# Kernel tuning notes

Hardware: AMD Instinct MI355X
Metric: run time of the kernel (lower is better)

## Reference

```python
import jax, jax.numpy as jnp
import numpy as np

B, T, F, E = 256, 256, 8, 128
H = 2 * E  # hidden_dim = 2*embedding_dim = 256
NL = 5     # num_layers per LSTM stack


def setup_inputs() -> dict:
    key = jax.random.key(0)
    ks = jax.random.split(key, 9)
    s1 = 1.0 / np.sqrt(H)
    s2 = 1.0 / np.sqrt(E)
    u = lambda k, shape, s: jax.random.uniform(k, shape, jnp.float32, -s, s)
    return {
        "x": jax.random.normal(ks[0], (B, T, F), jnp.float32),
        # stack 1: input F -> hidden H, 5 layers. b = b_ih + b_hh combined.
        "w_ih0_1": u(ks[1], (4 * H, F), s1),
        "w_ihr_1": u(ks[2], (NL - 1, 4 * H, H), s1),
        "w_hh_1": u(ks[3], (NL, 4 * H, H), s1),
        "b_1": u(ks[4], (NL, 4 * H), s1),
        # stack 2: input H -> hidden E, 5 layers
        "w_ih0_2": u(ks[5], (4 * E, H), s2),
        "w_ihr_2": u(ks[6], (NL - 1, 4 * E, E), s2),
        "w_hh_2": u(ks[7], (NL, 4 * E, E), s2),
        "b_2": u(ks[8], (NL, 4 * E), s2),
    }


def _lstm_layer(x, w_ih, w_hh, b):
    """x: [B,T,D] -> (outputs [B,T,Hd], final hidden [B,Hd]). PyTorch gate order i,f,g,o."""
    Hd = w_hh.shape[-1]
    # precompute input contribution for all timesteps (the big GEMM)
    xg = jnp.einsum('btd,gd->tbg', x, w_ih) + b  # [T,B,4Hd]
    h0 = jnp.zeros((x.shape[0], Hd), x.dtype)

    def step(carry, xt):
        h, c = carry
        g = xt + h @ w_hh.T
        i, f, gg, o = jnp.split(g, 4, axis=-1)
        c = jax.nn.sigmoid(f) * c + jax.nn.sigmoid(i) * jnp.tanh(gg)
        h = jax.nn.sigmoid(o) * jnp.tanh(c)
        return (h, c), h

    (h, _), hs = jax.lax.scan(step, (h0, h0), xg)
    return jnp.swapaxes(hs, 0, 1), h


def _stack(x, w_ih0, w_ihr, w_hh, b):
    y, h = _lstm_layer(x, w_ih0, w_hh[0], b[0])
    for l in range(1, w_hh.shape[0]):
        y, h = _lstm_layer(y, w_ihr[l - 1], w_hh[l], b[l])
    return y, h


def reference(x, w_ih0_1, w_ihr_1, w_hh_1, b_1, w_ih0_2, w_ihr_2, w_hh_2, b_2):
    x = x.reshape(x.shape[0], T, F)
    y, _ = _stack(x, w_ih0_1, w_ihr_1, w_hh_1, b_1)   # [B,T,H]
    _, h = _stack(y, w_ih0_2, w_ihr_2, w_hh_2, b_2)   # h: [B,E] last layer final hidden
    return h
```

## Files before the change

### kernel.cpp

```cpp
#include <hip/hip_runtime.h>
#include <math.h>

typedef unsigned short u16;
typedef unsigned int   u32;
typedef unsigned long long u64;
typedef __bf16 bf16x8 __attribute__((ext_vector_type(8)));
typedef float  f32x4  __attribute__((ext_vector_type(4)));

#define BB 256
#define TT 256
#define HD 256
#define ED 128
#define NSTEPS 265

#define H_U32   (10 * 2 * BB * HD)
#define CTR_OFF H_U32
#define CTR_U32 512
#define XP_OFF  (H_U32 + CTR_U32)
#define XP_U32  (BB * TT * 8)
#define WT_OFF  (XP_OFF + XP_U32)

__constant__ size_t g_woff[10] = {0ul,589824ul,1638400ul,2686976ul,3735552ul,
                                  4784128ul,5177344ul,5439488ul,5701632ul,5963776ul};
__constant__ int g_cb[11] = {0,73728,204800,335872,466944,598016,
                             647168,679936,712704,745472,778240};

__device__ __forceinline__ u16 f2bf_hi(float f) {
    u32 u = __float_as_uint(f);
    u32 r = (u + 0x7FFFu + ((u >> 16) & 1u)) >> 16;
    return (u16)r;
}
__device__ __forceinline__ float bf2f(u16 h) { return __uint_as_float(((u32)h) << 16); }
__device__ __forceinline__ float sigmoidf_(float v) { return 1.0f / (1.0f + expf(-v)); }

__global__ __launch_bounds__(256) void zero_state(u32* wsd) {
    const int n = XP_OFF;
    for (int i = blockIdx.x * blockDim.x + threadIdx.x; i < n; i += gridDim.x * blockDim.x)
        wsd[i] = 0u;
}

__global__ __launch_bounds__(256) void conv_x(const float* __restrict__ x, u32* __restrict__ wsd) {
    u32* xp = wsd + XP_OFF;
    for (int i = blockIdx.x * blockDim.x + threadIdx.x; i < XP_U32; i += gridDim.x * blockDim.x) {
        float v = x[i];
        u16 hi = f2bf_hi(v);
        u16 lo = f2bf_hi(v - bf2f(hi));
        xp[i] = (u32)hi | ((u32)lo << 16);
    }
}

__global__ __launch_bounds__(256) void conv_all(
    const float* __restrict__ w_ih0_1, const float* __restrict__ w_ihr_1,
    const float* __restrict__ w_hh_1,
    const float* __restrict__ w_ih0_2, const float* __restrict__ w_ihr_2,
    const float* __restrict__ w_hh_2,
    u32* __restrict__ wsd)
{
    __bf16* dst0 = (__bf16*)(wsd + WT_OFF);
    const int nch = 778240;
    for (int ci = blockIdx.x * blockDim.x + threadIdx.x; ci < nch;
         ci += gridDim.x * blockDim.x) {
        int l = 0;
        while (ci >= g_cb[l + 1]) ++l;
        int di = ci - g_cb[l];

        const int hd  = (l < 5) ? 256 : 128;
        const int din = (l == 0) ? 32 : ((l < 6) ? 256 : 128);
        const int xw  = (l == 0) ? 8 : din;
        const int Kp  = din + hd;
        const int nk  = Kp >> 5;

        const float *wih, *whh; int wihld, whhld;
        if (l == 0)      { wih = w_ih0_1;                                whh = w_hh_1;
                           wihld = 8;   whhld = 256; }
        else if (l < 5)  { wih = w_ihr_1 + (size_t)(l - 1) * 1024 * 256; whh = w_hh_1 + (size_t)l * 1024 * 256;
                           wihld = 256; whhld = 256; }
        else if (l == 5) { wih = w_ih0_2;                                whh = w_hh_2;
                           wihld = 256; whhld = 128; }
        else             { wih = w_ihr_2 + (size_t)(l - 6) * 512 * 128;  whh = w_hh_2 + (size_t)(l - 5) * 512 * 128;
                           wihld = 128; whhld = 128; }

        int lane = di & 63;
        int rem  = di >> 6;
        int kt   = rem % nk;
        int rem2 = rem / nk;
        int p    = rem2 & 1;
        int g    = (rem2 >> 1) & 3;
        int jt   = rem2 >> 3;
        int r15  = lane & 15, kq = lane >> 4;
        int row  = g * hd + jt * 16 + r15;

        bf16x8 o8;
        #pragma unroll
        for (int e = 0; e < 8; ++e) {
            int k = kt * 32 + kq * 8 + e;
            float v = 0.0f;
            if (k < xw) v = wih[(size_t)row * wihld + k];
            else if (k >= din && k < Kp) v = whh[(size_t)row * whhld + (k - din)];
            __bf16 h = (__bf16)v;
            o8[e] = p ? (__bf16)(v - (float)h) : h;
        }
        *(bf16x8*)(dst0 + g_woff[l] + (size_t)di * 8) = o8;
    }
}

__device__ __forceinline__ void unpack8(const uint4& a, const uint4& b, bf16x8& bh, bf16x8& bl) {
    union { u32 u[4]; bf16x8 v; } H, L;
    H.u[0] = (a.x & 0xFFFFu) | (a.y << 16);
    H.u[1] = (a.z & 0xFFFFu) | (a.w << 16);
    H.u[2] = (b.x & 0xFFFFu) | (b.y << 16);
    H.u[3] = (b.z & 0xFFFFu) | (b.w << 16);
    L.u[0] = (a.x >> 16) | (a.y & 0xFFFF0000u);
    L.u[1] = (a.z >> 16) | (a.w & 0xFFFF0000u);
    L.u[2] = (b.x >> 16) | (b.y & 0xFFFF0000u);
    L.u[3] = (b.z >> 16) | (b.w & 0xFFFF0000u);
    bh = H.v; bl = L.v;
}

template<int NKI, int NKT, bool ISL0>
__device__ void run_persist(int l, int bid, int xcd, int jt, int bt, int hd,
    const float* __restrict__ bias, u32* __restrict__ hbuf, u32* __restrict__ ctr,
    const u32* __restrict__ xp, float* __restrict__ out, const u16* __restrict__ A_sh)
{
    constexpr int DIN = NKI * 32;
    constexpr int RD  = (NKT < 8) ? NKT : 8;

    const int tid  = threadIdx.x;
    const int lane = tid & 63;
    const int wv   = tid >> 6;
    const int r15  = lane & 15;
    const int kq   = lane >> 4;
    const int brow = bt * 128 + wv * 16 + r15;
    const int j0   = jt * 16 + kq * 4;

    float bgr[4][4];
    #pragma unroll
    for (int g = 0; g < 4; ++g) {
        float4 v = *(const float4*)&bias[g * hd + j0];
        bgr[g][0] = v.x; bgr[g][1] = v.y; bgr[g][2] = v.z; bgr[g][3] = v.w;
    }

    int offH[4], offL[4];
    #pragma unroll
    for (int g = 0; g < 4; ++g) {
        offH[g] = (g * 2)     * NKT * 512 + lane * 8;
        offL[g] = (g * 2 + 1) * NKT * 512 + lane * 8;
    }

    float4 cv = make_float4(0.f, 0.f, 0.f, 0.f);
    const int lm = (l > 0) ? (l - 1) : 0;

    for (int w = 0; w < NSTEPS; ++w) {
        const int t = w - l;
        if (t >= 0 && t < TT) {
            const u32* hin   = hbuf + ((size_t)lm * 2 + (t & 1)) * (BB * HD);
            const u32* hprev = hbuf + ((size_t)l * 2 + ((t & 1) ^ 1)) * (BB * HD);
            u32*       hout  = hbuf + ((size_t)l * 2 + (t & 1)) * (BB * HD);

            auto ldB = [&](int kt, uint4& A, uint4& B) {
                if constexpr (ISL0) {
                    if (kt == 0) {
                        if (kq == 0) {
                            const uint4* p = (const uint4*)(xp + ((size_t)brow * TT + t) * 8);
                            A = p[0]; B = p[1];
                        } else { A = make_uint4(0,0,0,0); B = make_uint4(0,0,0,0); }
                    } else {
                        const u32* p = hprev + (size_t)brow * HD + (kt * 32 - 32) + kq * 8;
                        A = *(const uint4*)p; B = *(const uint4*)(p + 4);
                    }
                } else {
                    const int k0 = kt * 32 + kq * 8;
                    const u32* p = (kt < NKI) ? (hin + (size_t)brow * HD + k0)
                                              : (hprev + (size_t)brow * HD + (k0 - DIN));
                    A = *(const uint4*)p; B = *(const uint4*)(p + 4);
                }
            };

            f32x4 acc0 = {0.f,0.f,0.f,0.f}, acc1 = {0.f,0.f,0.f,0.f};
            f32x4 acc2 = {0.f,0.f,0.f,0.f}, acc3 = {0.f,0.f,0.f,0.f};

            uint4 rA[RD], rB[RD];
            #pragma unroll
            for (int i = 0; i < RD; ++i) ldB(i, rA[i], rB[i]);

            #pragma unroll
            for (int kt = 0; kt < NKT; ++kt) {
                bf16x8 bh, bl;
                unpack8(rA[kt % RD], rB[kt % RD], bh, bl);
                if (kt + RD < NKT) ldB(kt + RD, rA[kt % RD], rB[kt % RD]);

                const int kof = kt * 512;
                bf16x8 a0h = *(const bf16x8*)&A_sh[offH[0] + kof];
                bf16x8 a1h = *(const bf16x8*)&A_sh[offH[1] + kof];
                bf16x8 a2h = *(const bf16x8*)&A_sh[offH[2] + kof];
                bf16x8 a3h = *(const bf16x8*)&A_sh[offH[3] + kof];
                bf16x8 a0l = *(const bf16x8*)&A_sh[offL[0] + kof];
                bf16x8 a1l = *(const bf16x8*)&A_sh[offL[1] + kof];
                bf16x8 a2l = *(const bf16x8*)&A_sh[offL[2] + kof];
                bf16x8 a3l = *(const bf16x8*)&A_sh[offL[3] + kof];

                acc0 = __builtin_amdgcn_mfma_f32_16x16x32_bf16(a0h, bh, acc0, 0, 0, 0);
                acc1 = __builtin_amdgcn_mfma_f32_16x16x32_bf16(a1h, bh, acc1, 0, 0, 0);
                acc2 = __builtin_amdgcn_mfma_f32_16x16x32_bf16(a2h, bh, acc2, 0, 0, 0);
                acc3 = __builtin_amdgcn_mfma_f32_16x16x32_bf16(a3h, bh, acc3, 0, 0, 0);
                acc0 = __builtin_amdgcn_mfma_f32_16x16x32_bf16(a0h, bl, acc0, 0, 0, 0);
                acc1 = __builtin_amdgcn_mfma_f32_16x16x32_bf16(a1h, bl, acc1, 0, 0, 0);
                acc2 = __builtin_amdgcn_mfma_f32_16x16x32_bf16(a2h, bl, acc2, 0, 0, 0);
                acc3 = __builtin_amdgcn_mfma_f32_16x16x32_bf16(a3h, bl, acc3, 0, 0, 0);
                acc0 = __builtin_amdgcn_mfma_f32_16x16x32_bf16(a0l, bh, acc0, 0, 0, 0);
                acc1 = __builtin_amdgcn_mfma_f32_16x16x32_bf16(a1l, bh, acc1, 0, 0, 0);
                acc2 = __builtin_amdgcn_mfma_f32_16x16x32_bf16(a2l, bh, acc2, 0, 0, 0);
                acc3 = __builtin_amdgcn_mfma_f32_16x16x32_bf16(a3l, bh, acc3, 0, 0, 0);
            }

            float4 hv;
            {
                float i_, f_, g_, o_;
                i_ = sigmoidf_(acc0[0] + bgr[0][0]); f_ = sigmoidf_(acc1[0] + bgr[1][0]);
                g_ = tanhf   (acc2[0] + bgr[2][0]); o_ = sigmoidf_(acc3[0] + bgr[3][0]);
                cv.x = fmaf(f_, cv.x, i_ * g_); hv.x = o_ * tanhf(cv.x);
                i_ = sigmoidf_(acc0[1] + bgr[0][1]); f_ = sigmoidf_(acc1[1] + bgr[1][1]);
                g_ = tanhf   (acc2[1] + bgr[2][1]); o_ = sigmoidf_(acc3[1] + bgr[3][1]);
                cv.y = fmaf(f_, cv.y, i_ * g_); hv.y = o_ * tanhf(cv.y);
                i_ = sigmoidf_(acc0[2] + bgr[0][2]); f_ = sigmoidf_(acc1[2] + bgr[1][2]);
                g_ = tanhf   (acc2[2] + bgr[2][2]); o_ = sigmoidf_(acc3[2] + bgr[3][2]);
                cv.z = fmaf(f_, cv.z, i_ * g_); hv.z = o_ * tanhf(cv.z);
                i_ = sigmoidf_(acc0[3] + bgr[0][3]); f_ = sigmoidf_(acc1[3] + bgr[1][3]);
                g_ = tanhf   (acc2[3] + bgr[2][3]); o_ = sigmoidf_(acc3[3] + bgr[3][3]);
                cv.w = fmaf(f_, cv.w, i_ * g_); hv.w = o_ * tanhf(cv.w);
            }

            u32 pk0, pk1, pk2, pk3;
            {
                u16 h0 = f2bf_hi(hv.x); pk0 = (u32)h0 | ((u32)f2bf_hi(hv.x - bf2f(h0)) << 16);
                u16 h1 = f2bf_hi(hv.y); pk1 = (u32)h1 | ((u32)f2bf_hi(hv.y - bf2f(h1)) << 16);
                u16 h2 = f2bf_hi(hv.z); pk2 = (u32)h2 | ((u32)f2bf_hi(hv.z - bf2f(h2)) << 16);
                u16 h3 = f2bf_hi(hv.w); pk3 = (u32)h3 | ((u32)f2bf_hi(hv.w - bf2f(h3)) << 16);
            }
            u64* hp = (u64*)(hout + (size_t)brow * HD + j0);
            __hip_atomic_store(hp + 0, (u64)pk0 | ((u64)pk1 << 32), __ATOMIC_RELAXED, __HIP_MEMORY_SCOPE_AGENT);
            __hip_atomic_store(hp + 1, (u64)pk2 | ((u64)pk3 << 32), __ATOMIC_RELAXED, __HIP_MEMORY_SCOPE_AGENT);

            if (l == 9 && t == TT - 1)
                *(float4*)&out[(size_t)brow * ED + j0] = hv;
        }

        __syncthreads();
        if (tid == 0) {
            __hip_atomic_fetch_add(&ctr[xcd * 32], 1u,
                                   __ATOMIC_RELAXED, __HIP_MEMORY_SCOPE_AGENT);
            const u32 w1 = (u32)(w + 1);
            if (bid == 0) {
                for (int it = 0; it < (1 << 22); ++it) {
                    bool ok = true;
                    #pragma unroll
                    for (int r = 0; r < 8; ++r) {
                        u32 tgt = ((r == 7) ? 16u : 32u) * w1;
                        ok &= (__hip_atomic_load(&ctr[r * 32], __ATOMIC_RELAXED,
                                                 __HIP_MEMORY_SCOPE_AGENT) >= tgt);
                    }
                    if (ok) break;
                    __builtin_amdgcn_s_sleep(1);
                }
                __hip_atomic_store(&ctr[256], w1, __ATOMIC_RELAXED, __HIP_MEMORY_SCOPE_AGENT);
            } else {
                for (int it = 0; it < (1 << 22); ++it) {
                    if (__hip_atomic_load(&ctr[256], __ATOMIC_RELAXED,
                                          __HIP_MEMORY_SCOPE_AGENT) >= w1) break;
                    __builtin_amdgcn_s_sleep(1);
                }
            }
            __builtin_amdgcn_fence(__ATOMIC_ACQUIRE, "agent");
        }
        __syncthreads();
    }
}

__global__ __launch_bounds__(512, 2) void lstm_persist(
    const float* __restrict__ b_1, const float* __restrict__ b_2,
    u32* __restrict__ wsd, float* __restrict__ out)
{
    __shared__ __align__(16) u16 A_sh[65536];

    const int bid = blockIdx.x;
    const int xcd = bid & 7, slot = bid >> 3;
    int l, jt, bt;
    if (xcd < 5)      { l = xcd;               bt = slot >> 4;        jt = slot & 15; }
    else if (xcd == 5){ l = 5 + (slot >> 4);   bt = (slot >> 3) & 1;  jt = slot & 7; }
    else if (xcd == 6){ l = 7 + (slot >> 4);   bt = (slot >> 3) & 1;  jt = slot & 7; }
    else              { if (slot >= 16) return; l = 9; bt = slot >> 3; jt = slot & 7; }

    const int hd  = (l < 5) ? 256 : 128;
    const int din = (l == 0) ? 32 : ((l < 6) ? 256 : 128);
    const int nk  = (din + hd) >> 5;
    const float* bias = (l < 5) ? (b_1 + l * 1024) : (b_2 + (l - 5) * 512);

    u32* hbuf = wsd;
    u32* ctr  = wsd + CTR_OFF;
    const u32* xp = wsd + XP_OFF;
    const u16* wt = (const u16*)(wsd + WT_OFF);

    {
        const uint4* src = (const uint4*)(wt + g_woff[l] + (size_t)jt * 8 * nk * 512);
        uint4* dst = (uint4*)A_sh;
        const int n4 = nk * 512;
        for (int i = threadIdx.x; i < n4; i += 512) dst[i] = src[i];
    }
    __syncthreads();

    if (l == 0)
        run_persist<1, 9, true >(l, bid, xcd, jt, bt, hd, bias, hbuf, ctr, xp, out, A_sh);
    else if (l < 5)
        run_persist<8, 16, false>(l, bid, xcd, jt, bt, hd, bias, hbuf, ctr, xp, out, A_sh);
    else if (l == 5)
        run_persist<8, 12, false>(l, bid, xcd, jt, bt, hd, bias, hbuf, ctr, xp, out, A_sh);
    else
        run_persist<4, 8, false>(l, bid, xcd, jt, bt, hd, bias, hbuf, ctr, xp, out, A_sh);
}

extern "C" void kernel_launch(void* const* d_in, const int* in_sizes, int n_in,
                              void* d_out, int out_size, void* d_ws, size_t ws_size,
                              hipStream_t stream) {
    const float* x       = (const float*)d_in[0];
    const float* w_ih0_1 = (const float*)d_in[1];
    const float* w_ihr_1 = (const float*)d_in[2];
    const float* w_hh_1  = (const float*)d_in[3];
    const float* b_1     = (const float*)d_in[4];
    const float* w_ih0_2 = (const float*)d_in[5];
    const float* w_ihr_2 = (const float*)d_in[6];
    const float* w_hh_2  = (const float*)d_in[7];
    const float* b_2     = (const float*)d_in[8];
    u32*   wsd = (u32*)d_ws;
    float* out = (float*)d_out;

    hipLaunchKernelGGL(zero_state, dim3(1024), dim3(256), 0, stream, wsd);
    hipLaunchKernelGGL(conv_all, dim3(1024), dim3(256), 0, stream,
                       w_ih0_1, w_ihr_1, w_hh_1, w_ih0_2, w_ihr_2, w_hh_2, wsd);
    hipLaunchKernelGGL(conv_x, dim3(256), dim3(256), 0, stream, x, wsd);
    hipLaunchKernelGGL(lstm_persist, dim3(256), dim3(512), 0, stream,
                       b_1, b_2, wsd, out);
}
```

Before: 3.286 ms.

## Replace per-step global barrier with paired steps and per-group flag sync

Each global-barrier epoch now runs two timesteps per layer, with a lightweight per-(layer,batch-tile) group counter synchronising the blocks that share a recurrence between the two steps. The hidden-state ring buffer grows from depth 2 to 4 so that layers skewed by two steps can read inputs without overwriting them. The aim is to roughly halve the number of expensive grid-wide barriers. In exchange it adds a second sync point per epoch, deeper buffering in workspace, and a prefetch depth reduced from 8 to 4.

```diff
diff --git a/kernel.cpp b/kernel.cpp
--- a/kernel.cpp
+++ b/kernel.cpp
@@ -11,12 +11,13 @@
 #define TT 256
 #define HD 256
 #define ED 128
-#define NSTEPS 265
-
-#define H_U32   (10 * 2 * BB * HD)
+#define DEPTH 4
+#define NE 137
+
+#define H_U32   (10 * DEPTH * BB * HD)
 #define CTR_OFF H_U32
-#define CTR_U32 512
-#define XP_OFF  (H_U32 + CTR_U32)
+#define GRP_OFF (CTR_OFF + 512)
+#define XP_OFF  (GRP_OFF + 640)
 #define XP_U32  (BB * TT * 8)
 #define WT_OFF  (XP_OFF + XP_U32)
 
@@ -118,20 +119,21 @@
 }
 
 template<int NKI, int NKT, bool ISL0>
-__device__ void run_persist(int l, int bid, int xcd, int jt, int bt, int hd,
+__device__ void run_persist(int l, int bid, int xcd, int jt, int bt, int hd, u32 arr7,
+    int nblkg, u32* __restrict__ gflg,
     const float* __restrict__ bias, u32* __restrict__ hbuf, u32* __restrict__ ctr,
     const u32* __restrict__ xp, float* __restrict__ out, const u16* __restrict__ A_sh)
 {
     constexpr int DIN = NKI * 32;
-    constexpr int RD  = (NKT < 8) ? NKT : 8;
+    constexpr int RS  = (NKT < 4) ? NKT : 4;
 
     const int tid  = threadIdx.x;
     const int lane = tid & 63;
     const int wv   = tid >> 6;
     const int r15  = lane & 15;
-    const int kq   = lane >> 4;
+    const int kqc  = lane >> 4;
     const int brow = bt * 128 + wv * 16 + r15;
-    const int j0   = jt * 16 + kq * 4;
+    const int j0   = jt * 16 + kqc * 4;
 
     float bgr[4][4];
     #pragma unroll
@@ -150,112 +152,132 @@
     float4 cv = make_float4(0.f, 0.f, 0.f, 0.f);
     const int lm = (l > 0) ? (l - 1) : 0;
 
-    for (int w = 0; w < NSTEPS; ++w) {
-        const int t = w - l;
-        if (t >= 0 && t < TT) {
-            const u32* hin   = hbuf + ((size_t)lm * 2 + (t & 1)) * (BB * HD);
-            const u32* hprev = hbuf + ((size_t)l * 2 + ((t & 1) ^ 1)) * (BB * HD);
-            u32*       hout  = hbuf + ((size_t)l * 2 + (t & 1)) * (BB * HD);
-
-            auto ldB = [&](int kt, uint4& A, uint4& B) {
-                if constexpr (ISL0) {
-                    if (kt == 0) {
-                        if (kq == 0) {
-                            const uint4* p = (const uint4*)(xp + ((size_t)brow * TT + t) * 8);
-                            A = p[0]; B = p[1];
-                        } else { A = make_uint4(0,0,0,0); B = make_uint4(0,0,0,0); }
-                    } else {
-                        const u32* p = hprev + (size_t)brow * HD + (kt * 32 - 32) + kq * 8;
-                        A = *(const uint4*)p; B = *(const uint4*)(p + 4);
-                    }
+    auto STEP = [&](int t) {
+        const u32* hin   = hbuf + ((size_t)lm * DEPTH + (t & 3)) * (BB * HD);
+        const u32* hprev = hbuf + ((size_t)l * DEPTH + ((t - 1) & 3)) * (BB * HD);
+        u32*       hout  = hbuf + ((size_t)l * DEPTH + (t & 3)) * (BB * HD);
+
+        auto ldB = [&](int kt, uint4& A, uint4& B) {
+            if constexpr (ISL0) {
+                if (kt == 0) {
+                    if (kqc == 0) {
+                        const uint4* p = (const uint4*)(xp + ((size_t)brow * TT + t) * 8);
+                        A = p[0]; B = p[1];
+                    } else { A = make_uint4(0,0,0,0); B = make_uint4(0,0,0,0); }
                 } else {
-                    const int k0 = kt * 32 + kq * 8;
-                    const u32* p = (kt < NKI) ? (hin + (size_t)brow * HD + k0)
-                                              : (hprev + (size_t)brow * HD + (k0 - DIN));
+                    const u32* p = hprev + (size_t)brow * HD + (kt * 32 - 32) + kqc * 8;
                     A = *(const uint4*)p; B = *(const uint4*)(p + 4);
                 }
-            };
-
-            f32x4 acc0 = {0.f,0.f,0.f,0.f}, acc1 = {0.f,0.f,0.f,0.f};
-            f32x4 acc2 = {0.f,0.f,0.f,0.f}, acc3 = {0.f,0.f,0.f,0.f};
-
-            uint4 rA[RD], rB[RD];
-            #pragma unroll
-            for (int i = 0; i < RD; ++i) ldB(i, rA[i], rB[i]);
-
-            #pragma unroll
-            for (int kt = 0; kt < NKT; ++kt) {
-                bf16x8 bh, bl;
-                unpack8(rA[kt % RD], rB[kt % RD], bh, bl);
-                if (kt + RD < NKT) ldB(kt + RD, rA[kt % RD], rB[kt % RD]);
-
-                const int kof = kt * 512;
-                bf16x8 a0h = *(const bf16x8*)&A_sh[offH[0] + kof];
-                bf16x8 a1h = *(const bf16x8*)&A_sh[offH[1] + kof];
-                bf16x8 a2h = *(const bf16x8*)&A_sh[offH[2] + kof];
-                bf16x8 a3h = *(const bf16x8*)&A_sh[offH[3] + kof];
-                bf16x8 a0l = *(const bf16x8*)&A_sh[offL[0] + kof];
-                bf16x8 a1l = *(const bf16x8*)&A_sh[offL[1] + kof];
-                bf16x8 a2l = *(const bf16x8*)&A_sh[offL[2] + kof];
-                bf16x8 a3l = *(const bf16x8*)&A_sh[offL[3] + kof];
-
-                acc0 = __builtin_amdgcn_mfma_f32_16x16x32_bf16(a0h, bh, acc0, 0, 0, 0);
-                acc1 = __builtin_amdgcn_mfma_f32_16x16x32_bf16(a1h, bh, acc1, 0, 0, 0);
-                acc2 = __builtin_amdgcn_mfma_f32_16x16x32_bf16(a2h, bh, acc2, 0, 0, 0);
-                acc3 = __builtin_amdgcn_mfma_f32_16x16x32_bf16(a3h, bh, acc3, 0, 0, 0);
-                acc0 = __builtin_amdgcn_mfma_f32_16x16x32_bf16(a0h, bl, acc0, 0, 0, 0);
-                acc1 = __builtin_amdgcn_mfma_f32_16x16x32_bf16(a1h, bl, acc1, 0, 0, 0);
-                acc2 = __builtin_amdgcn_mfma_f32_16x16x32_bf16(a2h, bl, acc2, 0, 0, 0);
-                acc3 = __builtin_amdgcn_mfma_f32_16x16x32_bf16(a3h, bl, acc3, 0, 0, 0);
-                acc0 = __builtin_amdgcn_mfma_f32_16x16x32_bf16(a0l, bh, acc0, 0, 0, 0);
-                acc1 = __builtin_amdgcn_mfma_f32_16x16x32_bf16(a1l, bh, acc1, 0, 0, 0);
-                acc2 = __builtin_amdgcn_mfma_f32_16x16x32_bf16(a2l, bh, acc2, 0, 0, 0);
-                acc3 = __builtin_amdgcn_mfma_f32_16x16x32_bf16(a3l, bh, acc3, 0, 0, 0);
+            } else {
+                const int k0 = kt * 32 + kqc * 8;
+                const u32* p = (k0 < DIN) ? (hin + (size_t)brow * HD + k0)
+                                          : (hprev + (size_t)brow * HD + (k0 - DIN));
+                A = *(const uint4*)p; B = *(const uint4*)(p + 4);
             }
-
-            float4 hv;
-            {
-                float i_, f_, g_, o_;
-                i_ = sigmoidf_(acc0[0] + bgr[0][0]); f_ = sigmoidf_(acc1[0] + bgr[1][0]);
-                g_ = tanhf   (acc2[0] + bgr[2][0]); o_ = sigmoidf_(acc3[0] + bgr[3][0]);
-                cv.x = fmaf(f_, cv.x, i_ * g_); hv.x = o_ * tanhf(cv.x);
-                i_ = sigmoidf_(acc0[1] + bgr[0][1]); f_ = sigmoidf_(acc1[1] + bgr[1][1]);
-                g_ = tanhf   (acc2[1] + bgr[2][1]); o_ = sigmoidf_(acc3[1] + bgr[3][1]);
-                cv.y = fmaf(f_, cv.y, i_ * g_); hv.y = o_ * tanhf(cv.y);
-                i_ = sigmoidf_(acc0[2] + bgr[0][2]); f_ = sigmoidf_(acc1[2] + bgr[1][2]);
-                g_ = tanhf   (acc2[2] + bgr[2][2]); o_ = sigmoidf_(acc3[2] + bgr[3][2]);
-                cv.z = fmaf(f_, cv.z, i_ * g_); hv.z = o_ * tanhf(cv.z);
-                i_ = sigmoidf_(acc0[3] + bgr[0][3]); f_ = sigmoidf_(acc1[3] + bgr[1][3]);
-                g_ = tanhf   (acc2[3] + bgr[2][3]); o_ = sigmoidf_(acc3[3] + bgr[3][3]);
-                cv.w = fmaf(f_, cv.w, i_ * g_); hv.w = o_ * tanhf(cv.w);
+        };
+
+        f32x4 acc0 = {0.f,0.f,0.f,0.f}, acc1 = {0.f,0.f,0.f,0.f};
+        f32x4 acc2 = {0.f,0.f,0.f,0.f}, acc3 = {0.f,0.f,0.f,0.f};
+
+        uint4 ra[RS], rb[RS];
+        #pragma unroll
+        for (int i = 0; i < RS; ++i) ldB(i, ra[i], rb[i]);
+
+        #pragma unroll
+        for (int kt = 0; kt < NKT; ++kt) {
+            bf16x8 bh, bl;
+            unpack8(ra[kt % RS], rb[kt % RS], bh, bl);
+            if (kt + RS < NKT) ldB(kt + RS, ra[kt % RS], rb[kt % RS]);
+
+            const int kof = kt * 512;
+            bf16x8 a0h = *(const bf16x8*)&A_sh[offH[0] + kof];
+            bf16x8 a1h = *(const bf16x8*)&A_sh[offH[1] + kof];
+            bf16x8 a2h = *(const bf16x8*)&A_sh[offH[2] + kof];
+            bf16x8 a3h = *(const bf16x8*)&A_sh[offH[3] + kof];
+            bf16x8 a0l = *(const bf16x8*)&A_sh[offL[0] + kof];
+            bf16x8 a1l = *(const bf16x8*)&A_sh[offL[1] + kof];
+            bf16x8 a2l = *(const bf16x8*)&A_sh[offL[2] + kof];
+            bf16x8 a3l = *(const bf16x8*)&A_sh[offL[3] + kof];
+
+            acc0 = __builtin_amdgcn_mfma_f32_16x16x32_bf16(a0h, bh, acc0, 0, 0, 0);
+            acc1 = __builtin_amdgcn_mfma_f32_16x16x32_bf16(a1h, bh, acc1, 0, 0, 0);
+            acc2 = __builtin_amdgcn_mfma_f32_16x16x32_bf16(a2h, bh, acc2, 0, 0, 0);
+            acc3 = __builtin_amdgcn_mfma_f32_16x16x32_bf16(a3h, bh, acc3, 0, 0, 0);
+            acc0 = __builtin_amdgcn_mfma_f32_16x16x32_bf16(a0h, bl, acc0, 0, 0, 0);
+            acc1 = __builtin_amdgcn_mfma_f32_16x16x32_bf16(a1h, bl, acc1, 0, 0, 0);
+            acc2 = __builtin_amdgcn_mfma_f32_16x16x32_bf16(a2h, bl, acc2, 0, 0, 0);
+            acc3 = __builtin_amdgcn_mfma_f32_16x16x32_bf16(a3h, bl, acc3, 0, 0, 0);
+            acc0 = __builtin_amdgcn_mfma_f32_16x16x32_bf16(a0l, bh, acc0, 0, 0, 0);
+            acc1 = __builtin_amdgcn_mfma_f32_16x16x32_bf16(a1l, bh, acc1, 0, 0, 0);
+            acc2 = __builtin_amdgcn_mfma_f32_16x16x32_bf16(a2l, bh, acc2, 0, 0, 0);
+            acc3 = __builtin_amdgcn_mfma_f32_16x16x32_bf16(a3l, bh, acc3, 0, 0, 0);
+        }
+
+        float4 hv;
+        {
+            float i_, f_, g_, o_;
+            i_ = sigmoidf_(acc0[0] + bgr[0][0]); f_ = sigmoidf_(acc1[0] + bgr[1][0]);
+            g_ = tanhf   (acc2[0] + bgr[2][0]); o_ = sigmoidf_(acc3[0] + bgr[3][0]);
+            cv.x = fmaf(f_, cv.x, i_ * g_); hv.x = o_ * tanhf(cv.x);
+            i_ = sigmoidf_(acc0[1] + bgr[0][1]); f_ = sigmoidf_(acc1[1] + bgr[1][1]);
+            g_ = tanhf   (acc2[1] + bgr[2][1]); o_ = sigmoidf_(acc3[1] + bgr[3][1]);
+            cv.y = fmaf(f_, cv.y, i_ * g_); hv.y = o_ * tanhf(cv.y);
+            i_ = sigmoidf_(acc0[2] + bgr[0][2]); f_ = sigmoidf_(acc1[2] + bgr[1][2]);
+            g_ = tanhf   (acc2[2] + bgr[2][2]); o_ = sigmoidf_(acc3[2] + bgr[3][2]);
+            cv.z = fmaf(f_, cv.z, i_ * g_); hv.z = o_ * tanhf(cv.z);
+            i_ = sigmoidf_(acc0[3] + bgr[0][3]); f_ = sigmoidf_(acc1[3] + bgr[1][3]);
+            g_ = tanhf   (acc2[3] + bgr[2][3]); o_ = sigmoidf_(acc3[3] + bgr[3][3]);
+            cv.w = fmaf(f_, cv.w, i_ * g_); hv.w = o_ * tanhf(cv.w);
+        }
+
+        u32 pk0, pk1, pk2, pk3;
+        {
+            u16 h0 = f2bf_hi(hv.x); pk0 = (u32)h0 | ((u32)f2bf_hi(hv.x - bf2f(h0)) << 16);
+            u16 h1 = f2bf_hi(hv.y); pk1 = (u32)h1 | ((u32)f2bf_hi(hv.y - bf2f(h1)) << 16);
+            u16 h2 = f2bf_hi(hv.z); pk2 = (u32)h2 | ((u32)f2bf_hi(hv.z - bf2f(h2)) << 16);
+            u16 h3 = f2bf_hi(hv.w); pk3 = (u32)h3 | ((u32)f2bf_hi(hv.w - bf2f(h3)) << 16);
+        }
+        u64* hp = (u64*)(hout + (size_t)brow * HD + j0);
+        __hip_atomic_store(hp + 0, (u64)pk0 | ((u64)pk1 << 32), __ATOMIC_RELAXED, __HIP_MEMORY_SCOPE_AGENT);
+        __hip_atomic_store(hp + 1, (u64)pk2 | ((u64)pk3 << 32), __ATOMIC_RELAXED, __HIP_MEMORY_SCOPE_AGENT);
+
+        if (l == 9 && t == TT - 1)
+            *(float4*)&out[(size_t)brow * ED + j0] = hv;
+    };
+
+    for (int E = 0; E < NE; ++E) {
+        const int t0 = 2 * (E - l);
+        if (t0 >= 0 && t0 < TT) {
+            STEP(t0);
+            __syncthreads();
+            if (tid == 0)
+                __hip_atomic_fetch_add(gflg, 1u, __ATOMIC_RELAXED, __HIP_MEMORY_SCOPE_AGENT);
+        }
+        const int t1 = t0 + 1;
+        if (t1 >= 1 && t1 < TT) {
+            if (tid == 0) {
+                const u32 tg = (u32)nblkg * (u32)(E - l + 1);
+                for (int it = 0; it < (1 << 20); ++it) {
+                    if (__hip_atomic_load(gflg, __ATOMIC_RELAXED,
+                                          __HIP_MEMORY_SCOPE_AGENT) >= tg) break;
+                    __builtin_amdgcn_s_sleep(1);
+                }
             }
-
-            u32 pk0, pk1, pk2, pk3;
-            {
-                u16 h0 = f2bf_hi(hv.x); pk0 = (u32)h0 | ((u32)f2bf_hi(hv.x - bf2f(h0)) << 16);
-                u16 h1 = f2bf_hi(hv.y); pk1 = (u32)h1 | ((u32)f2bf_hi(hv.y - bf2f(h1)) << 16);
-                u16 h2 = f2bf_hi(hv.z); pk2 = (u32)h2 | ((u32)f2bf_hi(hv.z - bf2f(h2)) << 16);
-                u16 h3 = f2bf_hi(hv.w); pk3 = (u32)h3 | ((u32)f2bf_hi(hv.w - bf2f(h3)) << 16);
-            }
-            u64* hp = (u64*)(hout + (size_t)brow * HD + j0);
-            __hip_atomic_store(hp + 0, (u64)pk0 | ((u64)pk1 << 32), __ATOMIC_RELAXED, __HIP_MEMORY_SCOPE_AGENT);
-            __hip_atomic_store(hp + 1, (u64)pk2 | ((u64)pk3 << 32), __ATOMIC_RELAXED, __HIP_MEMORY_SCOPE_AGENT);
-
-            if (l == 9 && t == TT - 1)
-                *(float4*)&out[(size_t)brow * ED + j0] = hv;
+            __syncthreads();
+            STEP(t1);
         }
 
         __syncthreads();
         if (tid == 0) {
             __hip_atomic_fetch_add(&ctr[xcd * 32], 1u,
                                    __ATOMIC_RELAXED, __HIP_MEMORY_SCOPE_AGENT);
-            const u32 w1 = (u32)(w + 1);
+            const u32 w1 = (u32)(E + 1);
             if (bid == 0) {
                 for (int it = 0; it < (1 << 22); ++it) {
                     bool ok = true;
                     #pragma unroll
                     for (int r = 0; r < 8; ++r) {
-                        u32 tgt = ((r == 7) ? 16u : 32u) * w1;
+                        u32 tgt = ((r == 7) ? arr7 : 32u) * w1;
                         ok &= (__hip_atomic_load(&ctr[r * 32], __ATOMIC_RELAXED,
                                                  __HIP_MEMORY_SCOPE_AGENT) >= tgt);
                     }
@@ -294,11 +316,16 @@
     const int din = (l == 0) ? 32 : ((l < 6) ? 256 : 128);
     const int nk  = (din + hd) >> 5;
     const float* bias = (l < 5) ? (b_1 + l * 1024) : (b_2 + (l - 5) * 512);
+    const int nblkg = (l < 5) ? 32 : 16;
 
     u32* hbuf = wsd;
     u32* ctr  = wsd + CTR_OFF;
+    u32* gflg = wsd + GRP_OFF + (size_t)(l * 2 + bt) * 32;
     const u32* xp = wsd + XP_OFF;
     const u16* wt = (const u16*)(wsd + WT_OFF);
+
+    const int ng = (l < 5) ? 16 : 8;
+    (void)nblkg;
 
     {
         const uint4* src = (const uint4*)(wt + g_woff[l] + (size_t)jt * 8 * nk * 512);
@@ -309,13 +336,13 @@
     __syncthreads();
 
     if (l == 0)
-        run_persist<1, 9, true >(l, bid, xcd, jt, bt, hd, bias, hbuf, ctr, xp, out, A_sh);
+        run_persist<1, 9, true >(l, bid, xcd, jt, bt, hd, 16u, ng, gflg, bias, hbuf, ctr, xp, out, A_sh);
     else if (l < 5)
-        run_persist<8, 16, false>(l, bid, xcd, jt, bt, hd, bias, hbuf, ctr, xp, out, A_sh);
+        run_persist<8, 16, false>(l, bid, xcd, jt, bt, hd, 16u, ng, gflg, bias, hbuf, ctr, xp, out, A_sh);
     else if (l == 5)
-        run_persist<8, 12, false>(l, bid, xcd, jt, bt, hd, bias, hbuf, ctr, xp, out, A_sh);
+        run_persist<8, 12, false>(l, bid, xcd, jt, bt, hd, 16u, ng, gflg, bias, hbuf, ctr, xp, out, A_sh);
     else
-        run_persist<4, 8, false>(l, bid, xcd, jt, bt, hd, bias, hbuf, ctr, xp, out, A_sh);
+        run_persist<4, 8, false>(l, bid, xcd, jt, bt, hd, 16u, ng, gflg, bias, hbuf, ctr, xp, out, A_sh);
 }
 
 extern "C" void kernel_launch(void* const* d_in, const int* in_sizes, int n_in,
```

After: 2.998 ms. 1.1x faster.
